# Kernel tuning notes

Measured on AMD Instinct MI355X. Metric: run time of the kernel, lower is better.

The kernel has to match this reference:

```python
import jax, jax.numpy as jnp
import numpy as np
import math

B, H, N, D = 2, 8, 2048, 64

def setup_inputs() -> dict:
    key = jax.random.key(0)
    k1, k2, k3, k4, k5 = jax.random.split(key, 5)
    query = jax.random.normal(k1, (B, H, N, D), dtype=jnp.float32)
    k = jax.random.normal(k2, (B, H, N, D), dtype=jnp.float32)
    value = jax.random.normal(k3, (B, H, N, D), dtype=jnp.float32)
    mask = jax.random.randint(k4, (B, H, N, N), 0, 2, dtype=jnp.int32)
    p = jax.random.uniform(k5, (B, H, N, N), dtype=jnp.float32)
    return {"query": query, "key": k, "value": value, "mask": mask, "p": p}

def reference(query, key, value, mask, p):
    # scores: [B,H,N,N] = QK^T / sqrt(d)
    scores = jnp.einsum('bhqd,bhkd->bhqk', query, key) / math.sqrt(query.shape[-1])
    # additive log-probability bias
    scores = scores + jnp.log(p + 1e-12)
    # mask==0 -> -1e9
    scores = jnp.where(mask == 0, jnp.float32(-1e9), scores)
    p_attn = jax.nn.softmax(scores, axis=-1)
    out = jnp.einsum('bhqk,bhkd->bhqd', p_attn, value)
    return (out, p_attn)
```

## Files before the change

kernel.cpp:

```cpp
#include <hip/hip_runtime.h>


typedef float  f4v   __attribute__((ext_vector_type(4)));
typedef int    i4v   __attribute__((ext_vector_type(4)));
typedef __bf16 bf16x8 __attribute__((ext_vector_type(8)));
typedef unsigned short us8 __attribute__((ext_vector_type(8)));
typedef unsigned short us4 __attribute__((ext_vector_type(4)));
typedef unsigned int   u4v __attribute__((ext_vector_type(4)));
typedef _Float16       h2  __attribute__((ext_vector_type(2)));

#define MFMA16(a,b,c) __builtin_amdgcn_mfma_f32_16x16x32_bf16((a),(b),(c),0,0,0)

static __device__ __forceinline__ unsigned short f2bf(float f){
  unsigned u = __builtin_bit_cast(unsigned, f);
  u += 0x7fffu + ((u >> 16) & 1u);
  return (unsigned short)(u >> 16);
}
static __device__ __forceinline__ bf16x8 ldg8(const unsigned short* p){
  u4v v = *(const u4v*)p;
  return __builtin_bit_cast(bf16x8, v);
}

__global__ void prep_qk(const float* __restrict__ Q, const float* __restrict__ K,
                        unsigned short* __restrict__ Qb, unsigned short* __restrict__ Kb){
  int i = blockIdx.x * 256 + threadIdx.x;
  int base = i * 4;
  f4v q = *(const f4v*)(Q + base);
  f4v k = *(const f4v*)(K + base);
  us4 qo, ko;
#pragma unroll
  for(int j=0;j<4;j++){ qo[j] = f2bf(q[j] * 0.125f); ko[j] = f2bf(k[j]); }
  *(us4*)(Qb + base) = qo;
  *(us4*)(Kb + base) = ko;
}

__global__ void prep_vt(const float* __restrict__ V, unsigned short* __restrict__ Vt){
  __shared__ unsigned short tile[64][65];
  const int t  = threadIdx.x;
  const int bh = blockIdx.x >> 5;
  const int n0 = (blockIdx.x & 31) << 6;
  const int r  = t >> 2;
  const int c0 = (t & 3) << 4;
  const float* src = V + (((long)bh*2048 + n0 + r) << 6) + c0;
  f4v vv[4];
#pragma unroll
  for(int i=0;i<4;i++) vv[i] = *(const f4v*)(src + 4*i);
#pragma unroll
  for(int j=0;j<16;j++) tile[r][c0 + j] = f2bf(vv[j>>2][j&3]);
  __syncthreads();
  const int d  = t >> 2;
  const int n8 = (t & 3) << 4;
  us8 o0, o1;
#pragma unroll
  for(int j=0;j<8;j++){ o0[j] = tile[n8 + j][d]; o1[j] = tile[n8 + 8 + j][d]; }
  unsigned short* dst = Vt + (((long)bh*64 + d) << 11) + n0 + n8;
  *(us8*)dst       = o0;
  *(us8*)(dst + 8) = o1;
}

__global__ __launch_bounds__(512, 4) void attn_main(
    const float* __restrict__ P, const int* __restrict__ M,
    const unsigned short* __restrict__ Qb, const unsigned short* __restrict__ Kb,
    const unsigned short* __restrict__ Vt,
    float* __restrict__ out_o, float* __restrict__ out_p){

  __shared__ float shbuf[8448];
  __shared__ float wred[8][16];

  const int tid  = threadIdx.x;
  const int w    = tid >> 6;
  const int lane = tid & 63;
  const int m    = lane & 15;
  const int q    = lane >> 4;
  const int bidx = blockIdx.x;
  const int bh = ((bidx & 7) << 1) | ((bidx >> 3) & 1);
  const int qt = bidx >> 4;
  const int q0 = qt << 4;
  const int wbase = w << 8;

  const long  rowQ  = (long)bh*2048 + q0 + m;
  const long  pbase = rowQ * 2048;
  const unsigned short* Qrow = Qb + rowQ * 64;
  const bf16x8 qf0 = ldg8(Qrow + q*8);
  const bf16x8 qf1 = ldg8(Qrow + 32 + q*8);
  const unsigned short* Kbh = Kb + ((long)bh << 17);
  const unsigned short* Vbh = Vt + ((long)bh << 17);

  h2    eh[8][4];
  float l0 = 0.f, l1 = 0.f;
  float* st0 = shbuf + w * 1056;

#pragma unroll
  for(int c=0;c<8;c++){
    float* st = st0 + (c & 1) * 528;
    const int k0 = wbase + c*32;
    const unsigned short* Kp = Kbh + (long)(k0 + m)*64 + q*8;
    bf16x8 kf00 = ldg8(Kp);
    bf16x8 kf01 = ldg8(Kp + 32);
    bf16x8 kf10 = ldg8(Kp + 16*64);
    bf16x8 kf11 = ldg8(Kp + 16*64 + 32);
    const float* pp = P + pbase + k0 + q*8;
    f4v pv0 = *(const f4v*)pp;
    f4v pv1 = *(const f4v*)(pp + 4);
    const int* mp = M + pbase + k0 + q*8;
    i4v mv0 = *(const i4v*)mp;
    i4v mv1 = *(const i4v*)(mp + 4);

    f4v acc0 = {0.f,0.f,0.f,0.f}, acc1 = {0.f,0.f,0.f,0.f};
    acc0 = MFMA16(qf0, kf00, acc0);
    acc0 = MFMA16(qf1, kf01, acc0);
    acc1 = MFMA16(qf0, kf10, acc1);
    acc1 = MFMA16(qf1, kf11, acc1);

#pragma unroll
    for(int r=0;r<4;r++){
      st[(4*q + r)*33 + m]      = acc0[r];
      st[(4*q + r)*33 + 16 + m] = acc1[r];
    }
    float ev[8];
#pragma unroll
    for(int j=0;j<8;j++){
      float sv = st[m*33 + q*8 + j];
      float pj = (j < 4) ? pv0[j] : pv1[j-4];
      int   mj = (j < 4) ? mv0[j] : mv1[j-4];
      float e  = __expf(sv - 12.0f) * (pj + 1e-12f);
      e = (mj == 0) ? 0.f : e;
      if(j & 1) l1 += e; else l0 += e;
      ev[j] = e;
    }
#pragma unroll
    for(int i=0;i<4;i++){
      h2 t; t[0] = (_Float16)ev[2*i]; t[1] = (_Float16)ev[2*i+1];
      eh[c][i] = t;
    }
  }

  float l = l0 + l1;
  l += __shfl_xor(l, 16);
  l += __shfl_xor(l, 32);
  if(lane < 16) wred[w][lane] = l;
  __syncthreads();
  float L = 0.f;
#pragma unroll
  for(int i=0;i<8;i++) L += wred[i][m];
  const float rl = 1.0f / L;

  f4v o0={0.f,0.f,0.f,0.f}, o1={0.f,0.f,0.f,0.f}, o2={0.f,0.f,0.f,0.f}, o3={0.f,0.f,0.f,0.f};
#pragma unroll
  for(int c=0;c<8;c++){
    const int k0 = wbase + c*32;
    f4v w0v, w1v; us8 pb;
#pragma unroll
    for(int j=0;j<8;j++){
      float e  = (float)eh[c][j>>1][j&1];
      float pr = e * rl;
      if(j < 4) w0v[j] = pr; else w1v[j-4] = pr;
      pb[j] = f2bf(pr);
    }
    float* op = out_p + pbase + k0 + q*8;
    *(f4v*)op       = w0v;
    *(f4v*)(op + 4) = w1v;
    bf16x8 af = __builtin_bit_cast(bf16x8, pb);
    const unsigned short* Vp = Vbh + (long)m*2048 + k0 + q*8;
    o0 = MFMA16(af, ldg8(Vp),           o0);
    o1 = MFMA16(af, ldg8(Vp + 16*2048), o1);
    o2 = MFMA16(af, ldg8(Vp + 32*2048), o2);
    o3 = MFMA16(af, ldg8(Vp + 48*2048), o3);
  }

  float (*obuf)[16][64] = (float(*)[16][64])shbuf;
#pragma unroll
  for(int r=0;r<4;r++){
    obuf[w][4*q + r][m]      = o0[r];
    obuf[w][4*q + r][16 + m] = o1[r];
    obuf[w][4*q + r][32 + m] = o2[r];
    obuf[w][4*q + r][48 + m] = o3[r];
  }
  __syncthreads();
  if(tid < 256){
    const int row = tid >> 4, cg = (tid & 15) << 2;
    f4v s = {0.f,0.f,0.f,0.f};
#pragma unroll
    for(int i=0;i<8;i++) s += *(const f4v*)&obuf[i][row][cg];
    *(f4v*)(out_o + ((long)bh*2048 + q0 + row)*64 + cg) = s;
  }
}

extern "C" void kernel_launch(void* const* d_in, const int* in_sizes, int n_in,
                              void* d_out, int out_size, void* d_ws, size_t ws_size,
                              hipStream_t stream){
  const float* Q = (const float*)d_in[0];
  const float* K = (const float*)d_in[1];
  const float* V = (const float*)d_in[2];
  const int*   M = (const int*)  d_in[3];
  const float* P = (const float*)d_in[4];

  float* out_o = (float*)d_out;
  float* out_p = out_o + (size_t)2*8*2048*64;

  unsigned short* Qb = (unsigned short*)d_ws;
  unsigned short* Kb = Qb + (size_t)2*8*2048*64;
  unsigned short* Vt = Kb + (size_t)2*8*2048*64;

  prep_qk<<<2048, 256, 0, stream>>>(Q, K, Qb, Kb);
  prep_vt<<<512, 256, 0, stream>>>(V, Vt);
  attn_main<<<2048, 512, 0, stream>>>(P, M, Qb, Kb, Vt, out_o, out_p);
}
```

Before: 744.7 us.

## Coalesce P/mask loads and p_attn stores via LDS staging, transpose QK MFMA

```diff
diff --git a/kernel.cpp b/kernel.cpp
--- a/kernel.cpp
+++ b/kernel.cpp
@@ -8,6 +8,7 @@
 typedef unsigned short us4 __attribute__((ext_vector_type(4)));
 typedef unsigned int   u4v __attribute__((ext_vector_type(4)));
 typedef _Float16       h2  __attribute__((ext_vector_type(2)));
+typedef _Float16       h4  __attribute__((ext_vector_type(4)));
 
 #define MFMA16(a,b,c) __builtin_amdgcn_mfma_f32_16x16x32_bf16((a),(b),(c),0,0,0)
 
@@ -58,13 +59,15 @@
   *(us8*)(dst + 8) = o1;
 }
 
+#define PM_STRIDE 260
+
 __global__ __launch_bounds__(512, 4) void attn_main(
     const float* __restrict__ P, const int* __restrict__ M,
     const unsigned short* __restrict__ Qb, const unsigned short* __restrict__ Kb,
     const unsigned short* __restrict__ Vt,
     float* __restrict__ out_o, float* __restrict__ out_p){
 
-  __shared__ float shbuf[8448];
+  __shared__ __align__(16) _Float16 pmbuf[8][16*PM_STRIDE];
   __shared__ float wred[8][16];
 
   const int tid  = threadIdx.x;
@@ -78,55 +81,83 @@
   const int q0 = qt << 4;
   const int wbase = w << 8;
 
-  const long  rowQ  = (long)bh*2048 + q0 + m;
-  const long  pbase = rowQ * 2048;
+  _Float16* pmw = &pmbuf[w][0];
+
+  const int col4 = lane << 2;
+  const long g0 = ((long)bh*2048 + q0)*2048 + wbase + col4;
+
+  f4v pA0,pA1,pA2,pA3, pB0,pB1,pB2,pB3;
+  i4v mA0,mA1,mA2,mA3, mB0,mB1,mB2,mB3;
+
+#define P0_LOAD(s,g) \
+  p##s##0 = *(const f4v*)(P + g0 + ((g)*4+0)*2048); \
+  p##s##1 = *(const f4v*)(P + g0 + ((g)*4+1)*2048); \
+  p##s##2 = *(const f4v*)(P + g0 + ((g)*4+2)*2048); \
+  p##s##3 = *(const f4v*)(P + g0 + ((g)*4+3)*2048); \
+  m##s##0 = *(const i4v*)(M + g0 + ((g)*4+0)*2048); \
+  m##s##1 = *(const i4v*)(M + g0 + ((g)*4+1)*2048); \
+  m##s##2 = *(const i4v*)(M + g0 + ((g)*4+2)*2048); \
+  m##s##3 = *(const i4v*)(M + g0 + ((g)*4+3)*2048);
+
+#define P0_PROC1(pv, mv, r) { \
+  h4 hv; \
+  hv[0] = (mv[0]==0) ? (_Float16)0.f : (_Float16)pv[0]; \
+  hv[1] = (mv[1]==0) ? (_Float16)0.f : (_Float16)pv[1]; \
+  hv[2] = (mv[2]==0) ? (_Float16)0.f : (_Float16)pv[2]; \
+  hv[3] = (mv[3]==0) ? (_Float16)0.f : (_Float16)pv[3]; \
+  *(h4*)(pmw + (r)*PM_STRIDE + col4) = hv; }
+
+#define P0_PROC(s,g) \
+  P0_PROC1(p##s##0, m##s##0, (g)*4+0) \
+  P0_PROC1(p##s##1, m##s##1, (g)*4+1) \
+  P0_PROC1(p##s##2, m##s##2, (g)*4+2) \
+  P0_PROC1(p##s##3, m##s##3, (g)*4+3)
+
+  P0_LOAD(A,0)
+  P0_LOAD(B,1)
+  P0_PROC(A,0)
+  P0_LOAD(A,2)
+  P0_PROC(B,1)
+  P0_LOAD(B,3)
+  P0_PROC(A,2)
+  P0_PROC(B,3)
+
+  const long rowQ = (long)bh*2048 + q0 + m;
   const unsigned short* Qrow = Qb + rowQ * 64;
   const bf16x8 qf0 = ldg8(Qrow + q*8);
   const bf16x8 qf1 = ldg8(Qrow + 32 + q*8);
   const unsigned short* Kbh = Kb + ((long)bh << 17);
   const unsigned short* Vbh = Vt + ((long)bh << 17);
 
-  h2    eh[8][4];
+  h2 eh[8][4];
   float l0 = 0.f, l1 = 0.f;
-  float* st0 = shbuf + w * 1056;
 
 #pragma unroll
   for(int c=0;c<8;c++){
-    float* st = st0 + (c & 1) * 528;
-    const int k0 = wbase + c*32;
-    const unsigned short* Kp = Kbh + (long)(k0 + m)*64 + q*8;
+    const int k0l = c*32;
+    const int k0g = wbase + k0l;
+    const unsigned short* Kp = Kbh + (long)(k0g + m)*64 + q*8;
     bf16x8 kf00 = ldg8(Kp);
     bf16x8 kf01 = ldg8(Kp + 32);
     bf16x8 kf10 = ldg8(Kp + 16*64);
     bf16x8 kf11 = ldg8(Kp + 16*64 + 32);
-    const float* pp = P + pbase + k0 + q*8;
-    f4v pv0 = *(const f4v*)pp;
-    f4v pv1 = *(const f4v*)(pp + 4);
-    const int* mp = M + pbase + k0 + q*8;
-    i4v mv0 = *(const i4v*)mp;
-    i4v mv1 = *(const i4v*)(mp + 4);
 
     f4v acc0 = {0.f,0.f,0.f,0.f}, acc1 = {0.f,0.f,0.f,0.f};
-    acc0 = MFMA16(qf0, kf00, acc0);
-    acc0 = MFMA16(qf1, kf01, acc0);
-    acc1 = MFMA16(qf0, kf10, acc1);
-    acc1 = MFMA16(qf1, kf11, acc1);
-
+    acc0 = MFMA16(kf00, qf0, acc0);
+    acc0 = MFMA16(kf01, qf1, acc0);
+    acc1 = MFMA16(kf10, qf0, acc1);
+    acc1 = MFMA16(kf11, qf1, acc1);
+
+    h4 pmlo = *(const h4*)(pmw + m*PM_STRIDE + k0l + 4*q);
+    h4 pmhi = *(const h4*)(pmw + m*PM_STRIDE + k0l + 16 + 4*q);
+
+    float ev[8];
 #pragma unroll
     for(int r=0;r<4;r++){
-      st[(4*q + r)*33 + m]      = acc0[r];
-      st[(4*q + r)*33 + 16 + m] = acc1[r];
-    }
-    float ev[8];
-#pragma unroll
-    for(int j=0;j<8;j++){
-      float sv = st[m*33 + q*8 + j];
-      float pj = (j < 4) ? pv0[j] : pv1[j-4];
-      int   mj = (j < 4) ? mv0[j] : mv1[j-4];
-      float e  = __expf(sv - 12.0f) * (pj + 1e-12f);
-      e = (mj == 0) ? 0.f : e;
-      if(j & 1) l1 += e; else l0 += e;
-      ev[j] = e;
+      float e0 = (float)pmlo[r] * __expf(acc0[r] - 12.0f);
+      float e1 = (float)pmhi[r] * __expf(acc1[r] - 12.0f);
+      ev[r] = e0; ev[4+r] = e1;
+      l0 += e0; l1 += e1;
     }
 #pragma unroll
     for(int i=0;i<4;i++){
@@ -146,29 +177,64 @@
   const float rl = 1.0f / L;
 
   f4v o0={0.f,0.f,0.f,0.f}, o1={0.f,0.f,0.f,0.f}, o2={0.f,0.f,0.f,0.f}, o3={0.f,0.f,0.f,0.f};
+  const bool qodd = (q & 1) != 0;
+  const bool qmid = (q == 1) || (q == 2);
+
 #pragma unroll
   for(int c=0;c<8;c++){
-    const int k0 = wbase + c*32;
-    f4v w0v, w1v; us8 pb;
-#pragma unroll
-    for(int j=0;j<8;j++){
-      float e  = (float)eh[c][j>>1][j&1];
-      float pr = e * rl;
-      if(j < 4) w0v[j] = pr; else w1v[j-4] = pr;
-      pb[j] = f2bf(pr);
-    }
-    float* op = out_p + pbase + k0 + q*8;
-    *(f4v*)op       = w0v;
-    *(f4v*)(op + 4) = w1v;
+    const int k0l = c*32;
+    const int k0g = wbase + k0l;
+    float pr[8];
+#pragma unroll
+    for(int i=0;i<4;i++){
+      pr[2*i]   = (float)eh[c][i][0] * rl;
+      pr[2*i+1] = (float)eh[c][i][1] * rl;
+    }
+    h4 plo, phi;
+    plo[0]=(_Float16)pr[0]; plo[1]=(_Float16)pr[1]; plo[2]=(_Float16)pr[2]; plo[3]=(_Float16)pr[3];
+    phi[0]=(_Float16)pr[4]; phi[1]=(_Float16)pr[5]; phi[2]=(_Float16)pr[6]; phi[3]=(_Float16)pr[7];
+    *(h4*)(pmw + m*PM_STRIDE + k0l + 4*q)      = plo;
+    *(h4*)(pmw + m*PM_STRIDE + k0l + 16 + 4*q) = phi;
+
+    float s1_0,s1_1,s1_2,s1_3,s1_4,s1_5,s1_6,s1_7;
+    {
+      float t0=__shfl_xor(pr[0],16), t1=__shfl_xor(pr[1],16),
+            t2=__shfl_xor(pr[2],16), t3=__shfl_xor(pr[3],16),
+            t4=__shfl_xor(pr[4],16), t5=__shfl_xor(pr[5],16),
+            t6=__shfl_xor(pr[6],16), t7=__shfl_xor(pr[7],16);
+      s1_0 = qodd ? t4 : pr[0];  s1_1 = qodd ? t5 : pr[1];
+      s1_2 = qodd ? t6 : pr[2];  s1_3 = qodd ? t7 : pr[3];
+      s1_4 = qodd ? pr[4] : t0;  s1_5 = qodd ? pr[5] : t1;
+      s1_6 = qodd ? pr[6] : t2;  s1_7 = qodd ? pr[7] : t3;
+    }
+    us8 pb;
+    {
+      float u0=__shfl_xor(s1_0,48), u1=__shfl_xor(s1_1,48),
+            u2=__shfl_xor(s1_2,48), u3=__shfl_xor(s1_3,48),
+            u4=__shfl_xor(s1_4,48), u5=__shfl_xor(s1_5,48),
+            u6=__shfl_xor(s1_6,48), u7=__shfl_xor(s1_7,48);
+      pb[0] = f2bf(qmid ? u0 : s1_0);  pb[1] = f2bf(qmid ? u1 : s1_1);
+      pb[2] = f2bf(qmid ? u2 : s1_2);  pb[3] = f2bf(qmid ? u3 : s1_3);
+      pb[4] = f2bf(qmid ? u4 : s1_4);  pb[5] = f2bf(qmid ? u5 : s1_5);
+      pb[6] = f2bf(qmid ? u6 : s1_6);  pb[7] = f2bf(qmid ? u7 : s1_7);
+    }
     bf16x8 af = __builtin_bit_cast(bf16x8, pb);
-    const unsigned short* Vp = Vbh + (long)m*2048 + k0 + q*8;
+    const unsigned short* Vp = Vbh + (long)m*2048 + k0g + q*8;
     o0 = MFMA16(af, ldg8(Vp),           o0);
     o1 = MFMA16(af, ldg8(Vp + 16*2048), o1);
     o2 = MFMA16(af, ldg8(Vp + 32*2048), o2);
     o3 = MFMA16(af, ldg8(Vp + 48*2048), o3);
   }
 
-  float (*obuf)[16][64] = (float(*)[16][64])shbuf;
+#pragma unroll
+  for(int r=0;r<16;r++){
+    h4 v = *(const h4*)(pmw + r*PM_STRIDE + col4);
+    f4v ov; ov[0]=(float)v[0]; ov[1]=(float)v[1]; ov[2]=(float)v[2]; ov[3]=(float)v[3];
+    *(f4v*)(out_p + g0 + r*2048) = ov;
+  }
+
+  __syncthreads();
+  float (*obuf)[16][64] = (float(*)[16][64])&pmbuf[0][0];
 #pragma unroll
   for(int r=0;r<4;r++){
     obuf[w][4*q + r][m]      = o0[r];
```

New measurement: 708.2 us. 1.05x faster.

## Fuse PV MFMA into score loop with deferred normalization and shuffle-based transposes

Applied to the files above, without the earlier changes.

```diff
diff --git a/kernel.cpp b/kernel.cpp
--- a/kernel.cpp
+++ b/kernel.cpp
@@ -64,8 +64,8 @@
     const unsigned short* __restrict__ Vt,
     float* __restrict__ out_o, float* __restrict__ out_p){
 
-  __shared__ float shbuf[8448];
   __shared__ float wred[8][16];
+  __shared__ float obuf[8][16][64];
 
   const int tid  = threadIdx.x;
   const int w    = tid >> 6;
@@ -86,54 +86,90 @@
   const unsigned short* Kbh = Kb + ((long)bh << 17);
   const unsigned short* Vbh = Vt + ((long)bh << 17);
 
-  h2    eh[8][4];
+  const float* ppb = P + pbase + wbase + 4*q;
+  const int*   mpb = M + pbase + wbase + 4*q;
+
+  f4v pLA, pHA, pLB, pHB;
+  i4v mLA, mHA, mLB, mHB;
+  pLA = *(const f4v*)(ppb);
+  pHA = *(const f4v*)(ppb + 16);
+  mLA = *(const i4v*)(mpb);
+  mHA = *(const i4v*)(mpb + 16);
+
+  h2 eh[8][4];
   float l0 = 0.f, l1 = 0.f;
-  float* st0 = shbuf + w * 1056;
-
-#pragma unroll
-  for(int c=0;c<8;c++){
-    float* st = st0 + (c & 1) * 528;
-    const int k0 = wbase + c*32;
-    const unsigned short* Kp = Kbh + (long)(k0 + m)*64 + q*8;
-    bf16x8 kf00 = ldg8(Kp);
-    bf16x8 kf01 = ldg8(Kp + 32);
-    bf16x8 kf10 = ldg8(Kp + 16*64);
-    bf16x8 kf11 = ldg8(Kp + 16*64 + 32);
-    const float* pp = P + pbase + k0 + q*8;
-    f4v pv0 = *(const f4v*)pp;
-    f4v pv1 = *(const f4v*)(pp + 4);
-    const int* mp = M + pbase + k0 + q*8;
-    i4v mv0 = *(const i4v*)mp;
-    i4v mv1 = *(const i4v*)(mp + 4);
-
-    f4v acc0 = {0.f,0.f,0.f,0.f}, acc1 = {0.f,0.f,0.f,0.f};
-    acc0 = MFMA16(qf0, kf00, acc0);
-    acc0 = MFMA16(qf1, kf01, acc0);
-    acc1 = MFMA16(qf0, kf10, acc1);
-    acc1 = MFMA16(qf1, kf11, acc1);
-
-#pragma unroll
-    for(int r=0;r<4;r++){
-      st[(4*q + r)*33 + m]      = acc0[r];
-      st[(4*q + r)*33 + 16 + m] = acc1[r];
-    }
-    float ev[8];
-#pragma unroll
-    for(int j=0;j<8;j++){
-      float sv = st[m*33 + q*8 + j];
-      float pj = (j < 4) ? pv0[j] : pv1[j-4];
-      int   mj = (j < 4) ? mv0[j] : mv1[j-4];
-      float e  = __expf(sv - 12.0f) * (pj + 1e-12f);
-      e = (mj == 0) ? 0.f : e;
-      if(j & 1) l1 += e; else l0 += e;
-      ev[j] = e;
-    }
-#pragma unroll
-    for(int i=0;i<4;i++){
-      h2 t; t[0] = (_Float16)ev[2*i]; t[1] = (_Float16)ev[2*i+1];
-      eh[c][i] = t;
-    }
-  }
+  f4v o0={0.f,0.f,0.f,0.f}, o1={0.f,0.f,0.f,0.f}, o2={0.f,0.f,0.f,0.f}, o3={0.f,0.f,0.f,0.f};
+  const bool qodd = (q & 1) != 0;
+  const bool qmid = (q == 1) || (q == 2);
+
+#define CHUNK(c, CUR, NXT, cn) { \
+    const int k0g = wbase + (c)*32; \
+    const unsigned short* Kp = Kbh + (long)(k0g + m)*64 + q*8; \
+    bf16x8 kf00 = ldg8(Kp); \
+    bf16x8 kf01 = ldg8(Kp + 32); \
+    bf16x8 kf10 = ldg8(Kp + 16*64); \
+    bf16x8 kf11 = ldg8(Kp + 16*64 + 32); \
+    const unsigned short* Vp = Vbh + (long)m*2048 + k0g + q*8; \
+    bf16x8 vf0 = ldg8(Vp); \
+    bf16x8 vf1 = ldg8(Vp + 16*2048); \
+    bf16x8 vf2 = ldg8(Vp + 32*2048); \
+    bf16x8 vf3 = ldg8(Vp + 48*2048); \
+    pL##NXT = *(const f4v*)(ppb + (cn)*32); \
+    pH##NXT = *(const f4v*)(ppb + (cn)*32 + 16); \
+    mL##NXT = *(const i4v*)(mpb + (cn)*32); \
+    mH##NXT = *(const i4v*)(mpb + (cn)*32 + 16); \
+    f4v acc0 = {0.f,0.f,0.f,0.f}, acc1 = {0.f,0.f,0.f,0.f}; \
+    acc0 = MFMA16(kf00, qf0, acc0); \
+    acc0 = MFMA16(kf01, qf1, acc0); \
+    acc1 = MFMA16(kf10, qf0, acc1); \
+    acc1 = MFMA16(kf11, qf1, acc1); \
+    float ev0 = (mL##CUR[0]==0) ? 0.f : (pL##CUR[0] + 1e-12f) * __expf(acc0[0] - 12.0f); \
+    float ev1 = (mL##CUR[1]==0) ? 0.f : (pL##CUR[1] + 1e-12f) * __expf(acc0[1] - 12.0f); \
+    float ev2 = (mL##CUR[2]==0) ? 0.f : (pL##CUR[2] + 1e-12f) * __expf(acc0[2] - 12.0f); \
+    float ev3 = (mL##CUR[3]==0) ? 0.f : (pL##CUR[3] + 1e-12f) * __expf(acc0[3] - 12.0f); \
+    float ev4 = (mH##CUR[0]==0) ? 0.f : (pH##CUR[0] + 1e-12f) * __expf(acc1[0] - 12.0f); \
+    float ev5 = (mH##CUR[1]==0) ? 0.f : (pH##CUR[1] + 1e-12f) * __expf(acc1[1] - 12.0f); \
+    float ev6 = (mH##CUR[2]==0) ? 0.f : (pH##CUR[2] + 1e-12f) * __expf(acc1[2] - 12.0f); \
+    float ev7 = (mH##CUR[3]==0) ? 0.f : (pH##CUR[3] + 1e-12f) * __expf(acc1[3] - 12.0f); \
+    l0 += ev0 + ev2 + ev4 + ev6; \
+    l1 += ev1 + ev3 + ev5 + ev7; \
+    { h2 t; t[0]=(_Float16)ev0; t[1]=(_Float16)ev1; eh[(c)][0]=t; } \
+    { h2 t; t[0]=(_Float16)ev2; t[1]=(_Float16)ev3; eh[(c)][1]=t; } \
+    { h2 t; t[0]=(_Float16)ev4; t[1]=(_Float16)ev5; eh[(c)][2]=t; } \
+    { h2 t; t[0]=(_Float16)ev6; t[1]=(_Float16)ev7; eh[(c)][3]=t; } \
+    float t0=__shfl_xor(ev0,16), t1=__shfl_xor(ev1,16), \
+          t2=__shfl_xor(ev2,16), t3=__shfl_xor(ev3,16), \
+          t4=__shfl_xor(ev4,16), t5=__shfl_xor(ev5,16), \
+          t6=__shfl_xor(ev6,16), t7=__shfl_xor(ev7,16); \
+    float s10 = qodd ? t4 : ev0;  float s11 = qodd ? t5 : ev1; \
+    float s12 = qodd ? t6 : ev2;  float s13 = qodd ? t7 : ev3; \
+    float s14 = qodd ? ev4 : t0;  float s15 = qodd ? ev5 : t1; \
+    float s16 = qodd ? ev6 : t2;  float s17 = qodd ? ev7 : t3; \
+    float u0=__shfl_xor(s10,48), u1=__shfl_xor(s11,48), \
+          u2=__shfl_xor(s12,48), u3=__shfl_xor(s13,48), \
+          u4=__shfl_xor(s14,48), u5=__shfl_xor(s15,48), \
+          u6=__shfl_xor(s16,48), u7=__shfl_xor(s17,48); \
+    us8 pb; \
+    pb[0] = f2bf(qmid ? u0 : s10);  pb[1] = f2bf(qmid ? u1 : s11); \
+    pb[2] = f2bf(qmid ? u2 : s12);  pb[3] = f2bf(qmid ? u3 : s13); \
+    pb[4] = f2bf(qmid ? u4 : s14);  pb[5] = f2bf(qmid ? u5 : s15); \
+    pb[6] = f2bf(qmid ? u6 : s16);  pb[7] = f2bf(qmid ? u7 : s17); \
+    bf16x8 af = __builtin_bit_cast(bf16x8, pb); \
+    o0 = MFMA16(af, vf0, o0); \
+    o1 = MFMA16(af, vf1, o1); \
+    o2 = MFMA16(af, vf2, o2); \
+    o3 = MFMA16(af, vf3, o3); \
+  }
+
+  CHUNK(0, A, B, 1)
+  CHUNK(1, B, A, 2)
+  CHUNK(2, A, B, 3)
+  CHUNK(3, B, A, 4)
+  CHUNK(4, A, B, 5)
+  CHUNK(5, B, A, 6)
+  CHUNK(6, A, B, 7)
+  CHUNK(7, B, A, 7)
+#undef CHUNK
 
   float l = l0 + l1;
   l += __shfl_xor(l, 16);
@@ -145,30 +181,19 @@
   for(int i=0;i<8;i++) L += wred[i][m];
   const float rl = 1.0f / L;
 
-  f4v o0={0.f,0.f,0.f,0.f}, o1={0.f,0.f,0.f,0.f}, o2={0.f,0.f,0.f,0.f}, o3={0.f,0.f,0.f,0.f};
+  float* opb = out_p + pbase + wbase + 4*q;
 #pragma unroll
   for(int c=0;c<8;c++){
-    const int k0 = wbase + c*32;
-    f4v w0v, w1v; us8 pb;
-#pragma unroll
-    for(int j=0;j<8;j++){
-      float e  = (float)eh[c][j>>1][j&1];
-      float pr = e * rl;
-      if(j < 4) w0v[j] = pr; else w1v[j-4] = pr;
-      pb[j] = f2bf(pr);
+    f4v lo, hi;
+#pragma unroll
+    for(int i=0;i<4;i++){
+      lo[i] = (float)eh[c][i>>1][i&1] * rl;
+      hi[i] = (float)eh[c][(4+i)>>1][(4+i)&1] * rl;
     }
-    float* op = out_p + pbase + k0 + q*8;
-    *(f4v*)op       = w0v;
-    *(f4v*)(op + 4) = w1v;
-    bf16x8 af = __builtin_bit_cast(bf16x8, pb);
-    const unsigned short* Vp = Vbh + (long)m*2048 + k0 + q*8;
-    o0 = MFMA16(af, ldg8(Vp),           o0);
-    o1 = MFMA16(af, ldg8(Vp + 16*2048), o1);
-    o2 = MFMA16(af, ldg8(Vp + 32*2048), o2);
-    o3 = MFMA16(af, ldg8(Vp + 48*2048), o3);
-  }
-
-  float (*obuf)[16][64] = (float(*)[16][64])shbuf;
+    *(f4v*)(opb + c*32)      = lo;
+    *(f4v*)(opb + c*32 + 16) = hi;
+  }
+
 #pragma unroll
   for(int r=0;r<4;r++){
     obuf[w][4*q + r][m]      = o0[r];
@@ -182,6 +207,10 @@
     f4v s = {0.f,0.f,0.f,0.f};
 #pragma unroll
     for(int i=0;i<8;i++) s += *(const f4v*)&obuf[i][row][cg];
+    float Lr = 0.f;
+#pragma unroll
+    for(int i=0;i<8;i++) Lr += wred[i][row];
+    s *= (1.0f / Lr);
     *(f4v*)(out_o + ((long)bh*2048 + q0 + row)*64 + cg) = s;
   }
 }
```

New measurement: 717.4 us. 3.7% less time.
